# Optimization experiments

Measured on AMD Instinct MI355X. Metric: run time of the kernel, lower is better.

Reference implementation:

```python
import jax, jax.numpy as jnp
import numpy as np

N_HEAD = 16
D_MODEL = 1024
# c_attn compression metadata (coeff_ratio=0.25, 'medium')
ATTN_N = D_MODEL * 3 * D_MODEL          # 3145728
ATTN_PAD = 4194304                       # next pow2
ATTN_FFT = ATTN_PAD // 2 + 1             # 2097153
ATTN_KEEP = int(ATTN_FFT * 0.25)         # 524288
PROJ_N = D_MODEL * D_MODEL               # 1048576 (already pow2)
PROJ_PAD = PROJ_N
PROJ_FFT = PROJ_PAD // 2 + 1             # 524289
PROJ_KEEP = int(PROJ_FFT * 0.25)         # 131072


def setup_inputs() -> dict:
    key = jax.random.key(0)
    ks = jax.random.split(key, 9)
    B, S = 2, 2048
    x = jax.random.normal(ks[0], (B, S, D_MODEL), dtype=jnp.float32)
    c_attn_re = jax.random.normal(ks[1], (ATTN_KEEP,), dtype=jnp.float32)
    c_attn_im = jax.random.normal(ks[2], (ATTN_KEEP,), dtype=jnp.float32)
    # indices from topk are unique -> use a random permutation prefix
    c_attn_idx = jax.random.permutation(ks[3], ATTN_FFT)[:ATTN_KEEP].astype(jnp.int32)
    c_attn_scale = jnp.ones((1,), dtype=jnp.float32)
    c_proj_re = jax.random.normal(ks[4], (PROJ_KEEP,), dtype=jnp.float32)
    c_proj_im = jax.random.normal(ks[5], (PROJ_KEEP,), dtype=jnp.float32)
    c_proj_idx = jax.random.permutation(ks[6], PROJ_FFT)[:PROJ_KEEP].astype(jnp.int32)
    c_proj_scale = jnp.ones((1,), dtype=jnp.float32)
    c_attn_bias = jax.random.normal(ks[7], (3 * D_MODEL,), dtype=jnp.float32)
    c_proj_bias = jax.random.normal(ks[8], (D_MODEL,), dtype=jnp.float32)
    return dict(x=x, c_attn_re=c_attn_re, c_attn_im=c_attn_im, c_attn_idx=c_attn_idx,
                c_attn_scale=c_attn_scale, c_proj_re=c_proj_re, c_proj_im=c_proj_im,
                c_proj_idx=c_proj_idx, c_proj_scale=c_proj_scale,
                c_attn_bias=c_attn_bias, c_proj_bias=c_proj_bias)


def _decompress(re, im, idx, fft_len, pad_n, n, shape, scale):
    # zero-init + scatter of kept complex coeffs, then inverse rFFT
    full = jnp.zeros((fft_len,), dtype=jnp.complex64).at[idx].set(re + 1j * im)
    restored = jnp.fft.irfft(full, n=pad_n)[:n]
    return restored.reshape(shape) * scale[0]


def reference(x, c_attn_re, c_attn_im, c_attn_idx, c_attn_scale,
              c_proj_re, c_proj_im, c_proj_idx, c_proj_scale,
              c_attn_bias, c_proj_bias):
    Wa = _decompress(c_attn_re, c_attn_im, c_attn_idx, ATTN_FFT, ATTN_PAD,
                     ATTN_N, (D_MODEL, 3 * D_MODEL), c_attn_scale)
    Wp = _decompress(c_proj_re, c_proj_im, c_proj_idx, PROJ_FFT, PROJ_PAD,
                     PROJ_N, (D_MODEL, D_MODEL), c_proj_scale)
    B, S, _ = x.shape
    hd = D_MODEL // N_HEAD
    # F.linear(x, W.T, b) == x @ W + b  (Conv1D convention)
    qkv = x @ Wa + c_attn_bias                       # [B,S,3D]
    q, k, v = jnp.split(qkv, 3, axis=2)
    def heads(t):  # [B,S,D] -> [B,H,S,hd]
        return t.reshape(B, S, N_HEAD, hd).transpose(0, 2, 1, 3)
    q, k, v = heads(q), heads(k), heads(v)
    scores = jnp.einsum('bhqd,bhkd->bhqk', q, k) / jnp.sqrt(jnp.float32(hd))
    attn = jax.nn.softmax(scores, axis=-1)           # dropout = identity (eval)
    out = jnp.einsum('bhqk,bhkd->bhqd', attn, v)
    out = out.transpose(0, 2, 1, 3).reshape(B, S, D_MODEL)
    return out @ Wp + c_proj_bias
```

## Files before the change

kernel.cpp:

```cpp
#include <hip/hip_runtime.h>
#include <math.h>

#define N_HEADC  16
#define D_MODELC 1024
#define ATTN_N_C    3145728
#define ATTN_PAD_C  4194304
#define ATTN_NC     2097152
#define ATTN_KEEP_C 524288
#define PROJ_N_C    1048576
#define PROJ_PAD_C  1048576
#define PROJ_NC     524288
#define PROJ_KEEP_C 131072
#define BATCH_C 2
#define SEQ_C   2048

#define CEXP_C 0.18033688011112042f

typedef __attribute__((ext_vector_type(8))) short s16x8;
typedef __attribute__((ext_vector_type(4))) float f32x4;

#define AS1U(p) ((const __attribute__((address_space(1))) uint*)(p))
#define AS3U(p) ((__attribute__((address_space(3))) uint*)(p))

static __device__ __forceinline__ ushort f2bf(float f) {
    __bf16 b = (__bf16)f;
    return __builtin_bit_cast(ushort, b);
}
static __device__ __forceinline__ float bf2f(ushort u) {
    return __builtin_bit_cast(float, ((uint)u) << 16);
}
static __device__ __forceinline__ float2 cmul(float2 a, float2 b) {
    return make_float2(a.x * b.x - a.y * b.y, a.x * b.y + a.y * b.x);
}
static __device__ __forceinline__ float2 cadd(float2 a, float2 b) {
    return make_float2(a.x + b.x, a.y + b.y);
}
static __device__ __forceinline__ float2 csub(float2 a, float2 b) {
    return make_float2(a.x - b.x, a.y - b.y);
}
static __device__ __forceinline__ float2 crot(float2 z) {
    return make_float2(-z.y, z.x);
}

static __device__ __forceinline__ void r8core(const float2* a, float2* B) {
    const float2 t0 = cadd(a[0], a[4]), t1 = csub(a[0], a[4]);
    const float2 t2 = cadd(a[2], a[6]), t3 = csub(a[2], a[6]);
    const float2 t4 = cadd(a[1], a[5]), t5 = csub(a[1], a[5]);
    const float2 t6 = cadd(a[3], a[7]), t7 = csub(a[3], a[7]);
    const float2 E0 = cadd(t0, t2), E2 = csub(t0, t2);
    const float2 E1 = cadd(t1, crot(t3)), E3 = csub(t1, crot(t3));
    const float2 F0 = cadd(t4, t6), F2 = csub(t4, t6);
    const float2 F1 = cadd(t5, crot(t7)), F3 = csub(t5, crot(t7));
    const float c = 0.70710678118654752f;
    const float2 G1 = make_float2(c * (F1.x - F1.y), c * (F1.x + F1.y));
    const float2 G2 = crot(F2);
    const float2 G3 = make_float2(c * (-F3.x - F3.y), c * (F3.x - F3.y));
    B[0] = cadd(E0, F0); B[4] = csub(E0, F0);
    B[1] = cadd(E1, G1); B[5] = csub(E1, G1);
    B[2] = cadd(E2, G2); B[6] = csub(E2, G2);
    B[3] = cadd(E3, G3); B[7] = csub(E3, G3);
}


static __device__ __forceinline__ float2 pack_eval(
    const float2* __restrict__ H, int Nc, float th0, int k) {
    float2 g = H[k];
    float2 hm = H[Nc - k];
    if (k == 0) { g.y = 0.f; hm.y = 0.f; }
    float2 gh = make_float2(hm.x, -hm.y);
    float2 sum = make_float2(g.x + gh.x, g.y + gh.y);
    float2 dif = make_float2(g.x - gh.x, g.y - gh.y);
    float si, co;
    __sincosf(th0 * (float)k, &si, &co);
    float2 t = make_float2(dif.x * co - dif.y * si, dif.x * si + dif.y * co);
    return make_float2(sum.x - t.y, sum.y + t.x);
}

static __device__ __forceinline__ void r2_body(
    const float2* __restrict__ in, float2* __restrict__ out,
    int slog, int m, int half, int t) {
    if (t >= half) return;
    int s = 1 << slog;
    int q = t & (s - 1);
    int p = t >> slog;
    float si, co;
    __sincosf((float)(M_PI / (double)m) * (float)p, &si, &co);
    float2 a = in[q + s * p];
    float2 b = in[q + s * (p + m)];
    float2 su = cadd(a, b);
    float2 di = csub(a, b);
    int ob = q + ((s << 1) * p);
    out[ob]     = su;
    out[ob + s] = make_float2(di.x * co - di.y * si, di.x * si + di.y * co);
}

static __device__ __forceinline__ void r2_pack_body(
    const float2* __restrict__ H, float2* __restrict__ out,
    int Nc, float th0, int m, int half, int t) {
    if (t >= half) return;
    float2 a = pack_eval(H, Nc, th0, t);
    float2 b = pack_eval(H, Nc, th0, t + m);
    float si, co;
    __sincosf((float)(M_PI / (double)m) * (float)t, &si, &co);
    float2 su = cadd(a, b);
    float2 di = csub(a, b);
    out[2 * t]     = su;
    out[2 * t + 1] = make_float2(di.x * co - di.y * si, di.x * si + di.y * co);
}

static __device__ __forceinline__ void r8_body(
    const float2* __restrict__ in, float2* __restrict__ out,
    int slog, int M, float ang0, int eighth, int t) {
    if (t >= eighth) return;
    const int s = 1 << slog;
    const int q = t & (s - 1);
    const int p = t >> slog;
    float2 a[8];
#pragma unroll
    for (int j = 0; j < 8; ++j)
        a[j] = in[q + (size_t)s * (p + j * M)];
    float2 B[8];
    r8core(a, B);
    float si, co;
    __sincosf(ang0 * (float)p, &si, &co);
    const float2 w = make_float2(co, si);
    const int ob = q + 8 * s * p;
    out[ob] = B[0];
    float2 wj = w;
    out[ob + s] = cmul(wj, B[1]);
#pragma unroll
    for (int j = 2; j < 8; ++j) {
        wj = cmul(wj, w);
        out[ob + j * s] = cmul(wj, B[j]);
    }
}

static __device__ void r64_body(
    float2 (*Ysh)[8][9],
    const float2* __restrict__ in, float2* __restrict__ out,
    int slog, int M, int vb) {
    const int tid = threadIdx.x;
    const int g = tid & 31, u = tid >> 5;
    const int s = 1 << slog;
    const int M8 = M >> 3;
    const int G = vb * 32 + g;
    const int q = G & (s - 1);
    const int p0 = G >> slog;

    const int p = p0 + u * M8;
    float2 a[8];
#pragma unroll
    for (int j = 0; j < 8; ++j)
        a[j] = in[q + (size_t)s * (p + j * M)];
    float2 B[8];
    r8core(a, B);
    float si, co;
    __sincosf((0.78539816339744831f / (float)M) * (float)p, &si, &co);
    const float2 w = make_float2(co, si);
    Ysh[g][u][0] = B[0];
    float2 wj = w;
    Ysh[g][u][1] = cmul(wj, B[1]);
#pragma unroll
    for (int j = 2; j < 8; ++j) {
        wj = cmul(wj, w);
        Ysh[g][u][j] = cmul(wj, B[j]);
    }
    __syncthreads();

    float2 z[8];
#pragma unroll
    for (int jp = 0; jp < 8; ++jp)
        z[jp] = Ysh[g][jp][u];
    float2 B2[8];
    r8core(z, B2);
    __sincosf((0.78539816339744831f / (float)M8) * (float)p0, &si, &co);
    const float2 w2 = make_float2(co, si);
    const size_t ob = (size_t)q + (size_t)u * s + (size_t)64 * s * p0;
    out[ob] = B2[0];
    float2 wj2 = w2;
    out[ob + (size_t)8 * s] = cmul(wj2, B2[1]);
#pragma unroll
    for (int j2 = 2; j2 < 8; ++j2) {
        wj2 = cmul(wj2, w2);
        out[ob + (size_t)j2 * 8 * s] = cmul(wj2, B2[j2]);
    }
}

static __device__ void r64_pack_body(
    float2 (*Ysh)[8][9],
    const float2* __restrict__ H, float2* __restrict__ out,
    int Nc, float th0, int M, int vb) {
    const int tid = threadIdx.x;
    const int g = tid & 31, u = tid >> 5;
    const int M8 = M >> 3;
    const int p0 = vb * 32 + g;
    const int p = p0 + u * M8;
    float2 a[8];
#pragma unroll
    for (int j = 0; j < 8; ++j)
        a[j] = pack_eval(H, Nc, th0, p + j * M);
    float2 B[8];
    r8core(a, B);
    float si, co;
    __sincosf((0.78539816339744831f / (float)M) * (float)p, &si, &co);
    const float2 w = make_float2(co, si);
    Ysh[g][u][0] = B[0];
    float2 wj = w;
    Ysh[g][u][1] = cmul(wj, B[1]);
#pragma unroll
    for (int j = 2; j < 8; ++j) {
        wj = cmul(wj, w);
        Ysh[g][u][j] = cmul(wj, B[j]);
    }
    __syncthreads();

    float2 z[8];
#pragma unroll
    for (int jp = 0; jp < 8; ++jp)
        z[jp] = Ysh[g][jp][u];
    float2 B2[8];
    r8core(z, B2);
    __sincosf((0.78539816339744831f / (float)M8) * (float)p0, &si, &co);
    const float2 w2 = make_float2(co, si);
    const size_t ob = (size_t)u + (size_t)64 * p0;
    out[ob] = B2[0];
    float2 wj2 = w2;
    out[ob + 8] = cmul(wj2, B2[1]);
#pragma unroll
    for (int j2 = 2; j2 < 8; ++j2) {
        wj2 = cmul(wj2, w2);
        out[ob + (size_t)j2 * 8] = cmul(wj2, B2[j2]);
    }
}

static __device__ __forceinline__ void transpose_body(
    float (*T)[33], const float2* __restrict__ z, ushort* __restrict__ WT,
    int Kd, int Nd, float inv, const float* __restrict__ sc, int qcols, int vb) {
    const int nbx = Nd >> 5;
    const int n0 = (vb % nbx) * 32, k0 = (vb / nbx) * 32;
    const int tx = threadIdx.x & 31, ty = threadIdx.x >> 5;
    const float s = inv * sc[0];
    for (int r = ty; r < 32; r += 8) {
        size_t j = (size_t)(k0 + r) * Nd + n0 + tx;
        float2 zz = z[j >> 1];
        T[r][tx] = (j & 1) ? zz.y : zz.x;
    }
    __syncthreads();
    for (int r = ty; r < 32; r += 8) {
        const float fs = ((n0 + r) < qcols) ? s * CEXP_C : s;
        WT[(size_t)(n0 + r) * Kd + k0 + tx] = f2bf(T[tx][r] * fs);
    }
}


__global__ __launch_bounds__(256) void x_scatter(
    const float* __restrict__ x, ushort* __restrict__ xb,
    const float* __restrict__ re_a, const float* __restrict__ im_a,
    const int* __restrict__ idx_a, float2* __restrict__ Ha,
    const float* __restrict__ re_p, const float* __restrict__ im_p,
    const int* __restrict__ idx_p, float2* __restrict__ Hp) {
    const int B = blockIdx.x;
    if (B < 4096) {
        const int i = B * 256 + threadIdx.x;
        float4 v = *(const float4*)(x + (size_t)i * 4);
        ushort4 o;
        o.x = f2bf(v.x); o.y = f2bf(v.y); o.z = f2bf(v.z); o.w = f2bf(v.w);
        *(ushort4*)(xb + (size_t)i * 4) = o;
    } else {
        const int t = (B - 4096) * 256 + threadIdx.x;
        if (t < ATTN_KEEP_C) {
            Ha[idx_a[t]] = make_float2(re_a[t], im_a[t]);
        } else {
            const int u = t - ATTN_KEEP_C;
            Hp[idx_p[u]] = make_float2(re_p[u], im_p[u]);
        }
    }
}

__global__ __launch_bounds__(256) void fft_pack1(
    const float2* __restrict__ Ha, float2* __restrict__ oa, float tha, int na,
    const float2* __restrict__ Hp, float2* __restrict__ op, float thp,
    int mp, int halfp) {
    __shared__ float2 Ysh[32][8][9];
    if ((int)blockIdx.x < na)
        r64_pack_body(Ysh, Ha, oa, ATTN_NC, tha, ATTN_NC >> 3, blockIdx.x);
    else
        r2_pack_body(Hp, op, PROJ_NC, thp, mp, halfp,
                     (blockIdx.x - na) * 256 + threadIdx.x);
}

__global__ __launch_bounds__(256) void fft_r64_dual(
    const float2* __restrict__ ia, float2* __restrict__ oa, int sla, int Ma, int na,
    const float2* __restrict__ ip, float2* __restrict__ op, int slp, int Mp) {
    __shared__ float2 Ysh[32][8][9];
    if ((int)blockIdx.x < na)
        r64_body(Ysh, ia, oa, sla, Ma, blockIdx.x);
    else
        r64_body(Ysh, ip, op, slp, Mp, blockIdx.x - na);
}

__global__ __launch_bounds__(256) void fft_r8_r64(
    const float2* __restrict__ ia, float2* __restrict__ oa, int sla, float ang0,
    int eighth, int na,
    const float2* __restrict__ ip, float2* __restrict__ op, int slp, int Mp) {
    __shared__ float2 Ysh[32][8][9];
    if ((int)blockIdx.x < na)
        r8_body(ia, oa, sla, 1, ang0, eighth, (blockIdx.x) * 256 + threadIdx.x);
    else
        r64_body(Ysh, ip, op, slp, Mp, blockIdx.x - na);
}

__global__ __launch_bounds__(256) void transpose_dual(
    const float2* __restrict__ za, ushort* __restrict__ Wa, const float* __restrict__ sca,
    const float2* __restrict__ zp, ushort* __restrict__ Wp, const float* __restrict__ scp) {
    __shared__ float T[32][33];
    if (blockIdx.x < 3072)
        transpose_body(T, za, Wa, 1024, 3072, 1.f / ATTN_PAD_C, sca, 1024, blockIdx.x);
    else
        transpose_body(T, zp, Wp, 1024, 1024, 1.f / PROJ_PAD_C, scp, 0, blockIdx.x - 3072);
}

template <int OUTMODE>
__global__ __launch_bounds__(256) void gemm_bt_mfma(
    const ushort* __restrict__ A, const ushort* __restrict__ Bt,
    const float* __restrict__ bias, void* __restrict__ Cout,
    ushort* __restrict__ Vt, int M, int N, int K) {
    __shared__ ushort As[128 * 64];
    __shared__ ushort Bs[128 * 64];
    const int tid = threadIdx.x;
    const int wid = tid >> 6, lane = tid & 63, quad = lane >> 4, l16 = lane & 15;
    const int row0 = blockIdx.y * 128, col0 = blockIdx.x * 128;
    const int mh = (wid >> 1) * 64, nh = (wid & 1) * 64;
    const int r7 = l16 & 7;

    f32x4 acc[4][4] = {};

    for (int k0 = 0; k0 < K; k0 += 64) {
        __syncthreads();
#pragma unroll
        for (int rep = 0; rep < 4; ++rep) {
            int c = tid + rep * 256;
            int r = c >> 3;
            int kc = (c & 7) ^ (r & 7);
            ushort* lbA = &As[(rep * 256 + wid * 64) * 8];
            ushort* lbB = &Bs[(rep * 256 + wid * 64) * 8];
            __builtin_amdgcn_global_load_lds(
                AS1U(A + (size_t)(row0 + r) * K + k0 + kc * 8), AS3U(lbA), 16, 0, 0);
            __builtin_amdgcn_global_load_lds(
                AS1U(Bt + (size_t)(col0 + r) * K + k0 + kc * 8), AS3U(lbB), 16, 0, 0);
        }
        __syncthreads();
#pragma unroll
        for (int kk = 0; kk < 2; ++kk) {
            const int slot = ((kk * 4 + quad) ^ r7) * 8;
            s16x8 af[4], bfr[4];
#pragma unroll
            for (int mi = 0; mi < 4; ++mi)
                af[mi] = *(const s16x8*)&As[(mh + mi * 16 + l16) * 64 + slot];
#pragma unroll
            for (int ni = 0; ni < 4; ++ni)
                bfr[ni] = *(const s16x8*)&Bs[(nh + ni * 16 + l16) * 64 + slot];
#pragma unroll
            for (int mi = 0; mi < 4; ++mi)
#pragma unroll
                for (int ni = 0; ni < 4; ++ni)
                    acc[mi][ni] = __builtin_amdgcn_mfma_f32_16x16x32_bf16(
                        af[mi], bfr[ni], acc[mi][ni], 0, 0, 0);
        }
    }

#pragma unroll
    for (int mi = 0; mi < 4; ++mi)
#pragma unroll
        for (int ni = 0; ni < 4; ++ni) {
            const int col = col0 + nh + ni * 16 + l16;
            const int rbase = row0 + mh + mi * 16 + quad * 4;
            float bv = bias[col];
            if (OUTMODE == 1 && col < 1024) bv *= CEXP_C;
            if (OUTMODE == 0) {
                float* C = (float*)Cout;
#pragma unroll
                for (int j = 0; j < 4; ++j)
                    C[(size_t)(rbase + j) * N + col] = acc[mi][ni][j] + bv;
            } else {
                if (col < 2048) {
                    ushort* C = (ushort*)Cout;
#pragma unroll
                    for (int j = 0; j < 4; ++j)
                        C[(size_t)(rbase + j) * N + col] = f2bf(acc[mi][ni][j] + bv);
                } else {
                    const int bb = rbase >> 11;
                    const int seq = rbase & 2047;
                    const int d = col - 2048;
                    ushort4 pk;
                    pk.x = f2bf(acc[mi][ni][0] + bv);
                    pk.y = f2bf(acc[mi][ni][1] + bv);
                    pk.z = f2bf(acc[mi][ni][2] + bv);
                    pk.w = f2bf(acc[mi][ni][3] + bv);
                    *(ushort4*)&Vt[(size_t)bb * 2097152 + (size_t)d * 2048 + seq] = pk;
                }
            }
        }
}

__global__ __launch_bounds__(256, 3) void attn_fwd_mfma(
    const ushort* __restrict__ qkv, const ushort* __restrict__ Vt,
    ushort* __restrict__ Op, float* __restrict__ Lp) {
    const int L = blockIdx.x;
    const int xcd = L & 7, slot = L >> 3;
    const int g = xcd * 4 + (slot >> 5);
    const int within = slot & 31;
    const int b = g >> 4, h = g & 15;
    const int qb = within >> 1, split = within & 1;
    const int tid = threadIdx.x;
    const int wid = tid >> 6, lane = tid & 63, quad = lane >> 4, l16 = lane & 15;
    const int wq = wid * 32;
    const int kt0 = split * 16;
    const int r7 = l16 & 7;

    __shared__ ushort Ks[2][64 * 64];
    __shared__ ushort Vts[2][64 * 64];
    __shared__ ushort Ps[128 * 64];

#pragma unroll
    for (int rep = 0; rep < 4; ++rep) {
        int c = tid + rep * 256;
        int r = c >> 3;
        int kc = (c & 7) ^ (r & 7);
        ushort* lb = &Ps[(rep * 256 + wid * 64) * 8];
        __builtin_amdgcn_global_load_lds(
            AS1U(qkv + (size_t)(b * 2048 + qb * 128 + r) * 3072 + h * 64 + kc * 8),
            AS3U(lb), 16, 0, 0);
    }
    __syncthreads();

    s16x8 qreg[2][2];
#pragma unroll
    for (int ks = 0; ks < 2; ++ks) {
        const int slot2 = ((ks * 4 + quad) ^ r7) * 8;
#pragma unroll
        for (int ni = 0; ni < 2; ++ni)
            qreg[ks][ni] = *(const s16x8*)&Ps[(wq + ni * 16 + l16) * 64 + slot2];
    }

    f32x4 o[4][2] = {};
    float l_r[2] = {0.f, 0.f};

    for (int tt = 0; tt < 16; tt += 2) {
        __syncthreads();
#pragma unroll
        for (int half = 0; half < 2; ++half) {
            const int kt = kt0 + tt + half;
#pragma unroll
            for (int rep = 0; rep < 2; ++rep) {
                int c = tid + rep * 256;
                int r = c >> 3;
                int kc = (c & 7) ^ (r & 7);
                ushort* lbK = &Ks[half][(rep * 256 + wid * 64) * 8];
                ushort* lbV = &Vts[half][(rep * 256 + wid * 64) * 8];
                __builtin_amdgcn_global_load_lds(
                    AS1U(qkv + (size_t)(b * 2048 + kt * 64 + r) * 3072 + 1024 + h * 64 + kc * 8),
                    AS3U(lbK), 16, 0, 0);
                __builtin_amdgcn_global_load_lds(
                    AS1U(Vt + (size_t)b * 2097152 + (size_t)(h * 64 + r) * 2048 + kt * 64 + kc * 8),
                    AS3U(lbV), 16, 0, 0);
            }
        }
        __syncthreads();

#pragma unroll
        for (int half = 0; half < 2; ++half) {
            f32x4 s[4][2] = {};
#pragma unroll
            for (int ks = 0; ks < 2; ++ks) {
                const int slot2 = ((ks * 4 + quad) ^ r7) * 8;
                s16x8 ka[4];
#pragma unroll
                for (int mi = 0; mi < 4; ++mi)
                    ka[mi] = *(const s16x8*)&Ks[half][(mi * 16 + l16) * 64 + slot2];
#pragma unroll
                for (int mi = 0; mi < 4; ++mi)
#pragma unroll
                    for (int ni = 0; ni < 2; ++ni)
                        s[mi][ni] = __builtin_amdgcn_mfma_f32_16x16x32_bf16(
                            ka[mi], qreg[ks][ni], s[mi][ni], 0, 0, 0);
            }

#pragma unroll
            for (int ni = 0; ni < 2; ++ni)
#pragma unroll
                for (int mi = 0; mi < 4; ++mi) {
                    ushort4 pk;
#pragma unroll
                    for (int j = 0; j < 4; ++j) {
                        float p = exp2f(s[mi][ni][j]);
                        l_r[ni] += p;
                        ((ushort*)&pk)[j] = f2bf(p);
                    }
                    const int jq = 2 * mi + (quad >> 1);
                    *(ushort4*)&Ps[(wq + ni * 16 + l16) * 64 + ((jq ^ r7)) * 8 + (quad & 1) * 4] = pk;
                }

#pragma unroll
            for (int ks = 0; ks < 2; ++ks) {
                const int slot2 = ((ks * 4 + quad) ^ r7) * 8;
                s16x8 va[4], pb[2];
#pragma unroll
                for (int md = 0; md < 4; ++md)
                    va[md] = *(const s16x8*)&Vts[half][(md * 16 + l16) * 64 + slot2];
#pragma unroll
                for (int ni = 0; ni < 2; ++ni)
                    pb[ni] = *(const s16x8*)&Ps[(wq + ni * 16 + l16) * 64 + slot2];
#pragma unroll
                for (int md = 0; md < 4; ++md)
#pragma unroll
                    for (int ni = 0; ni < 2; ++ni)
                        o[md][ni] = __builtin_amdgcn_mfma_f32_16x16x32_bf16(
                            va[md], pb[ni], o[md][ni], 0, 0, 0);
            }
        }
    }

#pragma unroll
    for (int ni = 0; ni < 2; ++ni) {
        float l = l_r[ni];
        l += __shfl_xor(l, 16);
        l += __shfl_xor(l, 32);
        const size_t row = (size_t)(b * 2048 + qb * 128 + wq + ni * 16 + l16);
        if (quad == 0)
            Lp[(size_t)split * 65536 + row * 16 + h] = l;
#pragma unroll
        for (int md = 0; md < 4; ++md) {
            ushort4 pk;
#pragma unroll
            for (int j = 0; j < 4; ++j)
                ((ushort*)&pk)[j] = f2bf(o[md][ni][j]);
            *(ushort4*)&Op[(size_t)split * 4194304 + row * 1024 + h * 64 + md * 16 + quad * 4] = pk;
        }
    }
}

__global__ __launch_bounds__(256) void attn_reduce(
    const ushort* __restrict__ Op, const float* __restrict__ Lp,
    ushort* __restrict__ ctx) {
    const int i = blockIdx.x * 256 + threadIdx.x;
    const size_t base = (size_t)i * 4;
    const int row = (int)(base >> 10);
    const int hh = (int)((base & 1023) >> 6);
    const float l = Lp[row * 16 + hh] + Lp[65536 + row * 16 + hh];
    const float inv = 1.f / l;
    ushort4 a = *(const ushort4*)&Op[base];
    ushort4 b = *(const ushort4*)&Op[4194304 + base];
    ushort4 o;
    o.x = f2bf((bf2f(a.x) + bf2f(b.x)) * inv);
    o.y = f2bf((bf2f(a.y) + bf2f(b.y)) * inv);
    o.z = f2bf((bf2f(a.z) + bf2f(b.z)) * inv);
    o.w = f2bf((bf2f(a.w) + bf2f(b.w)) * inv);
    *(ushort4*)&ctx[base] = o;
}

extern "C" void kernel_launch(void* const* d_in, const int* in_sizes, int n_in,
                              void* d_out, int out_size, void* d_ws, size_t ws_size,
                              hipStream_t stream) {
    const float* x        = (const float*)d_in[0];
    const float* attn_re  = (const float*)d_in[1];
    const float* attn_im  = (const float*)d_in[2];
    const int*   attn_idx = (const int*)d_in[3];
    const float* attn_sc  = (const float*)d_in[4];
    const float* proj_re  = (const float*)d_in[5];
    const float* proj_im  = (const float*)d_in[6];
    const int*   proj_idx = (const int*)d_in[7];
    const float* proj_sc  = (const float*)d_in[8];
    const float* attn_b   = (const float*)d_in[9];
    const float* proj_b   = (const float*)d_in[10];
    float* out = (float*)d_out;

    const size_t MB = 1048576;
    char* w = (char*)d_ws;
    float2* A0  = (float2*)(w);
    float2* A1  = (float2*)(w + 16 * MB);
    float2* Ha  = (float2*)(w + 32 * MB);
    float2* Hp  = (float2*)(w + 49 * MB);
    float2* P0  = (float2*)(w + 54 * MB);
    float2* P1  = (float2*)(w + 58 * MB);
    ushort* WaT = (ushort*)(w + 62 * MB);
    ushort* WpT = (ushort*)(w + 68 * MB);
    ushort* x_bf= (ushort*)(w + 70 * MB);
    ushort* qkvb= (ushort*)(w);
    ushort* Vt  = (ushort*)(w + 24 * MB);
    ushort* ctx = (ushort*)(w + 32 * MB);
    ushort* Op  = (ushort*)(w + 40 * MB);
    float*  Lp  = (float*)(w + 56 * MB);

    hipMemsetAsync(w + 32 * MB, 0, 22 * MB, stream);

    x_scatter<<<6656, 256, 0, stream>>>(
        x, x_bf, attn_re, attn_im, attn_idx, Ha, proj_re, proj_im, proj_idx, Hp);

    fft_pack1<<<2048, 256, 0, stream>>>(
        Ha, A1, (float)(2.0 * M_PI / ATTN_PAD_C), 1024,
        Hp, P1, (float)(2.0 * M_PI / PROJ_PAD_C), PROJ_NC / 2, PROJ_NC / 2);

    fft_r64_dual<<<1280, 256, 0, stream>>>(A1, A0, 6,  ATTN_NC >> 9,  1024,
                                           P1, P0, 1,  PROJ_NC >> 4);
    fft_r64_dual<<<1280, 256, 0, stream>>>(A0, A1, 12, ATTN_NC >> 15, 1024,
                                           P0, P1, 7,  PROJ_NC >> 10);
    fft_r8_r64 <<<1280, 256, 0, stream>>>(A1, A0, 18, (float)(M_PI / 4.0),
                                          ATTN_NC / 8, 1024,
                                          P1, P0, 13, PROJ_NC >> 16);
    transpose_dual<<<4096, 256, 0, stream>>>(A0, WaT, attn_sc, P0, WpT, proj_sc);

    gemm_bt_mfma<1><<<dim3(3072 / 128, 4096 / 128), 256, 0, stream>>>(
        x_bf, WaT, attn_b, qkvb, Vt, 4096, 3072, 1024);

    attn_fwd_mfma<<<1024, 256, 0, stream>>>(qkvb, Vt, Op, Lp);
    attn_reduce<<<4096, 256, 0, stream>>>(Op, Lp, ctx);

    gemm_bt_mfma<0><<<dim3(1024 / 128, 4096 / 128), 256, 0, stream>>>(
        ctx, WpT, proj_b, out, (ushort*)nullptr, 4096, 1024, 1024);
}
```

Measured before the change: 263.5 us.

## Drop split-K attention and reduce kernel, normalize in attention epilogue

The attention kernel no longer splits the key sequence into two halves written as partial outputs. Each block now loops over all 32 key tiles and normalizes by the row sum in its epilogue, writing ctx directly. This removes the separate reduce kernel, its launch, and the round trip of bf16 partials through global memory. In exchange the grid halves to 512 blocks, so occupancy and parallelism across the GPU drop.

Measured after the change: 262.5 us. About the same (-0.4%).

```diff
diff --git a/kernel.cpp b/kernel.cpp
--- a/kernel.cpp
+++ b/kernel.cpp
@@ -405,17 +405,15 @@
 
 __global__ __launch_bounds__(256, 3) void attn_fwd_mfma(
     const ushort* __restrict__ qkv, const ushort* __restrict__ Vt,
-    ushort* __restrict__ Op, float* __restrict__ Lp) {
+    ushort* __restrict__ ctx) {
     const int L = blockIdx.x;
     const int xcd = L & 7, slot = L >> 3;
-    const int g = xcd * 4 + (slot >> 5);
-    const int within = slot & 31;
+    const int g = xcd * 4 + (slot >> 4);
+    const int qb = slot & 15;
     const int b = g >> 4, h = g & 15;
-    const int qb = within >> 1, split = within & 1;
     const int tid = threadIdx.x;
     const int wid = tid >> 6, lane = tid & 63, quad = lane >> 4, l16 = lane & 15;
     const int wq = wid * 32;
-    const int kt0 = split * 16;
     const int r7 = l16 & 7;
 
     __shared__ ushort Ks[2][64 * 64];
@@ -446,11 +444,11 @@
     f32x4 o[4][2] = {};
     float l_r[2] = {0.f, 0.f};
 
-    for (int tt = 0; tt < 16; tt += 2) {
+    for (int tt = 0; tt < 32; tt += 2) {
         __syncthreads();
 #pragma unroll
         for (int half = 0; half < 2; ++half) {
-            const int kt = kt0 + tt + half;
+            const int kt = tt + half;
 #pragma unroll
             for (int rep = 0; rep < 2; ++rep) {
                 int c = tid + rep * 256;
@@ -526,37 +524,17 @@
         float l = l_r[ni];
         l += __shfl_xor(l, 16);
         l += __shfl_xor(l, 32);
+        const float inv = 1.f / l;
         const size_t row = (size_t)(b * 2048 + qb * 128 + wq + ni * 16 + l16);
-        if (quad == 0)
-            Lp[(size_t)split * 65536 + row * 16 + h] = l;
 #pragma unroll
         for (int md = 0; md < 4; ++md) {
             ushort4 pk;
 #pragma unroll
             for (int j = 0; j < 4; ++j)
-                ((ushort*)&pk)[j] = f2bf(o[md][ni][j]);
-            *(ushort4*)&Op[(size_t)split * 4194304 + row * 1024 + h * 64 + md * 16 + quad * 4] = pk;
-        }
-    }
-}
-
-__global__ __launch_bounds__(256) void attn_reduce(
-    const ushort* __restrict__ Op, const float* __restrict__ Lp,
-    ushort* __restrict__ ctx) {
-    const int i = blockIdx.x * 256 + threadIdx.x;
-    const size_t base = (size_t)i * 4;
-    const int row = (int)(base >> 10);
-    const int hh = (int)((base & 1023) >> 6);
-    const float l = Lp[row * 16 + hh] + Lp[65536 + row * 16 + hh];
-    const float inv = 1.f / l;
-    ushort4 a = *(const ushort4*)&Op[base];
-    ushort4 b = *(const ushort4*)&Op[4194304 + base];
-    ushort4 o;
-    o.x = f2bf((bf2f(a.x) + bf2f(b.x)) * inv);
-    o.y = f2bf((bf2f(a.y) + bf2f(b.y)) * inv);
-    o.z = f2bf((bf2f(a.z) + bf2f(b.z)) * inv);
-    o.w = f2bf((bf2f(a.w) + bf2f(b.w)) * inv);
-    *(ushort4*)&ctx[base] = o;
+                ((ushort*)&pk)[j] = f2bf(o[md][ni][j] * inv);
+            *(ushort4*)&ctx[row * 1024 + h * 64 + md * 16 + quad * 4] = pk;
+        }
+    }
 }
 
 extern "C" void kernel_launch(void* const* d_in, const int* in_sizes, int n_in,
@@ -589,8 +567,6 @@
     ushort* qkvb= (ushort*)(w);
     ushort* Vt  = (ushort*)(w + 24 * MB);
     ushort* ctx = (ushort*)(w + 32 * MB);
-    ushort* Op  = (ushort*)(w + 40 * MB);
-    float*  Lp  = (float*)(w + 56 * MB);
 
     hipMemsetAsync(w + 32 * MB, 0, 22 * MB, stream);
 
@@ -613,8 +589,7 @@
     gemm_bt_mfma<1><<<dim3(3072 / 128, 4096 / 128), 256, 0, stream>>>(
         x_bf, WaT, attn_b, qkvb, Vt, 4096, 3072, 1024);
 
-    attn_fwd_mfma<<<1024, 256, 0, stream>>>(qkvb, Vt, Op, Lp);
-    attn_reduce<<<4096, 256, 0, stream>>>(Op, Lp, ctx);
+    attn_fwd_mfma<<<512, 256, 0, stream>>>(qkvb, Vt, ctx);
 
     gemm_bt_mfma<0><<<dim3(1024 / 128, 4096 / 128), 256, 0, stream>>>(
         ctx, WpT, proj_b, out, (ushort*)nullptr, 4096, 1024, 1024);
```
